# Performance work log

Measured on AMD Instinct MI355X. Metric: run time of the kernel, lower is better.

## Reference

```python
import jax, jax.numpy as jnp
import numpy as np

N_NODES = 100000
N_EDGES = 1600000
F_IN, HIDDEN, N_CLS = 128, 128, 40


def _gcn_layer(h, W, b, src, dst, norm, n):
    # h: [n, d_in] -> linear transform then edge-normalized scatter-add
    h = h @ W                                   # [n, d_out]
    msg = h[src] * norm[:, None]                # gather over edges [E', d_out]
    out = jax.ops.segment_sum(msg, dst, num_segments=n)
    return out + b


def setup_inputs() -> dict:
    key = jax.random.key(0)
    k1, k2, k3, k4 = jax.random.split(key, 4)
    x = jax.random.normal(k1, (N_NODES, F_IN), dtype=jnp.float32)
    edge_index = jax.random.randint(k2, (2, N_EDGES), 0, N_NODES, dtype=jnp.int32)
    # glorot-style init
    W1 = jax.random.normal(k3, (F_IN, HIDDEN), dtype=jnp.float32) * (1.0 / np.sqrt(F_IN))
    W2 = jax.random.normal(k4, (HIDDEN, N_CLS), dtype=jnp.float32) * (1.0 / np.sqrt(HIDDEN))
    b1 = jnp.zeros((HIDDEN,), dtype=jnp.float32)
    b2 = jnp.zeros((N_CLS,), dtype=jnp.float32)
    return {"x": x, "edge_index": edge_index, "W1": W1, "b1": b1,
            "W2": W2, "b2": b2, "dropout": 0}


def reference(x, edge_index, W1, b1, W2, b2, dropout):
    n = x.shape[0]
    src, dst = edge_index[0], edge_index[1]
    # add self loops (PyG GCNConv default)
    loop = jnp.arange(n, dtype=src.dtype)
    src = jnp.concatenate([src, loop])
    dst = jnp.concatenate([dst, loop])
    # symmetric normalization D^{-1/2} (A+I) D^{-1/2}
    deg = jax.ops.segment_sum(jnp.ones(src.shape, dtype=x.dtype), dst, num_segments=n)
    dinv = jnp.where(deg > 0, jax.lax.rsqrt(deg), 0.0)
    norm = dinv[src] * dinv[dst]                # [E + n]
    h = jax.nn.relu(_gcn_layer(x, W1, b1, src, dst, norm, n))
    # F.dropout with training=False is identity (eval mode)
    return _gcn_layer(h, W2, b2, src, dst, norm, n)
```

## Files before the change

kernel.cpp:

```cpp
#include <hip/hip_runtime.h>
#include <stdint.h>


#define NF 128
#define NC 40
#define PSHIFT 7
#define PNODES 128
#define GH 256

typedef __attribute__((ext_vector_type(8))) short short8;
typedef __attribute__((ext_vector_type(4))) float float4m;

__device__ __forceinline__ float bflo2f(unsigned int u) {
  union { unsigned int i; float f; } v; v.i = u << 16; return v.f;
}
__device__ __forceinline__ float bfhi2f(unsigned int u) {
  union { unsigned int i; float f; } v; v.i = u & 0xffff0000u; return v.f;
}
__device__ __forceinline__ unsigned short f2bf(float f) {
  union { float f; unsigned int i; } v; v.f = f;
  unsigned int x = v.i;
  return (unsigned short)((x + 0x7fffu + ((x >> 16) & 1u)) >> 16);
}

__device__ __forceinline__ unsigned int rowld64(const unsigned int* __restrict__ B,
                                                int idx, int lane) {
  unsigned int off = ((unsigned)idx << 6) | (unsigned)lane;
  __builtin_assume(off < (1u << 25));
  return B[off];
}
__device__ __forceinline__ unsigned int rowld20(const unsigned int* __restrict__ B,
                                                int idx, int ci) {
  unsigned int off = (unsigned)idx * 20u + (unsigned)ci;
  __builtin_assume(off < (1u << 22));
  return B[off];
}
__device__ __forceinline__ int4 bidx4(const int4* __restrict__ B, int off) {
  __builtin_assume(off >= 0 && off < (1 << 22));
  return B[off];
}

__global__ __launch_bounds__(256) void hist_pack_k(
    const int* __restrict__ ei, int* __restrict__ histT, int E, int CPB, int NPART,
    const float* __restrict__ W1, const float* __restrict__ W2,
    unsigned short* __restrict__ Bpack, unsigned short* __restrict__ W2pack,
    unsigned int* __restrict__ Hsu, unsigned int* __restrict__ H2u, int n) {
  int tid = threadIdx.x, bid = blockIdx.x;
  if (bid >= GH) {
    int g = (bid - GH) * 256 + tid;
    const float* W; unsigned short* dst; int cols, frag;
    if (g < 2048)      { W = W1; dst = Bpack;  cols = 128; frag = g; }
    else if (g < 2816) { W = W2; dst = W2pack; cols = 40;  frag = g - 2048; }
    else if (g < 2880) { Hsu[(size_t)n * 64 + (g - 2816)] = 0u; return; }
    else if (g < 2900) { H2u[(size_t)n * 20 + (g - 2880)] = 0u; return; }
    else return;
    int ct = frag >> 8, ks = (frag >> 6) & 3, lane = frag & 63;
    int quad = lane >> 4, l15 = lane & 15;
    int col = ct * 16 + l15, krow = ks * 32 + quad * 8;
    ushort4 lo = {0,0,0,0}, hi = {0,0,0,0};
    if (col < cols) {
      lo.x = f2bf(W[(krow + 0) * cols + col]);
      lo.y = f2bf(W[(krow + 1) * cols + col]);
      lo.z = f2bf(W[(krow + 2) * cols + col]);
      lo.w = f2bf(W[(krow + 3) * cols + col]);
      hi.x = f2bf(W[(krow + 4) * cols + col]);
      hi.y = f2bf(W[(krow + 5) * cols + col]);
      hi.z = f2bf(W[(krow + 6) * cols + col]);
      hi.w = f2bf(W[(krow + 7) * cols + col]);
    }
    *(ushort4*)&dst[(size_t)frag * 8 + 0] = lo;
    *(ushort4*)&dst[(size_t)frag * 8 + 4] = hi;
    return;
  }
  __shared__ int h[1024];
  for (int i = tid; i < NPART; i += 256) h[i] = 0;
  __syncthreads();
  int e0 = bid * CPB, e1 = min(e0 + CPB, E);
  for (int e = e0 + tid; e < e1; e += 256)
    atomicAdd(&h[ei[E + e] >> PSHIFT], 1);
  __syncthreads();
  for (int i = tid; i < NPART; i += 256) histT[(size_t)i * GH + bid] = h[i];
}

__global__ __launch_bounds__(256) void scanA_k(int* __restrict__ histT,
                                               int* __restrict__ partTotal) {
  __shared__ int sm[GH];
  int tid = threadIdx.x, p = blockIdx.x;
  int v = histT[(size_t)p * GH + tid];
  sm[tid] = v; __syncthreads();
  for (int off = 1; off < GH; off <<= 1) {
    int t = (tid >= off) ? sm[tid - off] : 0;
    __syncthreads();
    sm[tid] += t;
    __syncthreads();
  }
  histT[(size_t)p * GH + tid] = sm[tid] - v;
  if (tid == GH - 1) partTotal[p] = sm[GH - 1];
}

__global__ __launch_bounds__(1024) void scanB_k(const int* __restrict__ partTotal,
                                                int* __restrict__ base, int NPART) {
  __shared__ int sm[1024];
  int tid = threadIdx.x;
  int v = (tid < NPART) ? partTotal[tid] : 0;
  sm[tid] = v; __syncthreads();
  for (int off = 1; off < 1024; off <<= 1) {
    int t = (tid >= off) ? sm[tid - off] : 0;
    __syncthreads();
    sm[tid] += t;
    __syncthreads();
  }
  if (tid < NPART) base[tid] = sm[tid] - v;
}

__global__ __launch_bounds__(256) void scatter_k(const int* __restrict__ ei,
                                                 const int* __restrict__ histT,
                                                 const int* __restrict__ base,
                                                 unsigned int* __restrict__ epart,
                                                 int E, int CPB, int NPART) {
  __shared__ int off[1024];
  int tid = threadIdx.x, bid = blockIdx.x;
  for (int i = tid; i < NPART; i += 256)
    off[i] = base[i] + histT[(size_t)i * GH + bid];
  __syncthreads();
  int e0 = bid * CPB, e1 = min(e0 + CPB, E);
  for (int e = e0 + tid; e < e1; e += 256) {
    int s = ei[e], d = ei[E + e];
    int pos = atomicAdd(&off[d >> PSHIFT], 1);
    epart[pos] = ((unsigned int)(d & (PNODES - 1)) << 25) | (unsigned int)s;
  }
}

__global__ __launch_bounds__(256) void degpart_k(const unsigned int* __restrict__ epart,
                                                 const int* __restrict__ base,
                                                 const int* __restrict__ partTotal,
                                                 int* __restrict__ deg,
                                                 float* __restrict__ dinv, int n) {
  __shared__ int lcnt[PNODES];
  int tid = threadIdx.x, p = blockIdx.x;
  if (tid < PNODES) lcnt[tid] = 0;
  __syncthreads();
  int st = base[p], m = partTotal[p];
  for (int e = tid; e < m; e += 256)
    atomicAdd(&lcnt[epart[(size_t)st + e] >> 25], 1);
  __syncthreads();
  int node = (p << PSHIFT) + tid;
  if (tid < PNODES && node < n) {
    int c = lcnt[tid];
    deg[node] = c;
    dinv[node] = rsqrtf((float)c + 1.0f);
  }
}

__global__ __launch_bounds__(256) void build_gemm_k(
    const float* __restrict__ x, const unsigned short* __restrict__ Bpack,
    unsigned short* __restrict__ Hs, const unsigned int* __restrict__ epart,
    const int* __restrict__ base, const int* __restrict__ partTotal,
    const float* __restrict__ dinv,
    int* __restrict__ bucket, int n, int NPART, int G1) {
  __shared__ alignas(16) char smem[50176];
  int tid = threadIdx.x, bid = blockIdx.x;

  if (bid % 3 == 2) {
    int pidx = bid / 3;
    if (pidx >= NPART) return;
    int* lcnt = (int*)smem;
    int* lbuck = lcnt + PNODES;
    if (tid < PNODES) lcnt[tid] = 0;
    __syncthreads();
    int st = base[pidx], m = partTotal[pidx];
    for (int e = tid; e < m; e += 256) {
      unsigned int u = epart[(size_t)st + e];
      int ln = (int)(u >> 25), s = (int)(u & 0x1ffffffu);
      int pos = atomicAdd(&lcnt[ln], 1);
      if (pos < 64) lbuck[ln * 64 + pos] = s;
    }
    __syncthreads();
    int node0 = pidx << PSHIFT;
    int nn = min(PNODES, n - node0);
    for (int i = tid; i < nn; i += 256) {
      int c = lcnt[i]; if (c > 64) c = 64;
      int c8 = (c + 7) & ~7; if (c8 > 64) c8 = 64;
      for (int p = c; p < c8; p++) lbuck[i * 64 + p] = n;
    }
    __syncthreads();
    int4* bg = (int4*)&bucket[(size_t)node0 * 64];
    const int4* bl = (const int4*)lbuck;
    for (int i = tid; i < nn * 16; i += 256) {
      int nd = i >> 4, q = i & 15;
      int c = lcnt[nd]; if (c > 64) c = 64;
      int c8 = (c + 7) & ~7; if (c8 > 64) c8 = 64;
      if (q * 4 < c8) bg[i] = bl[i];
    }
    return;
  }

  int idx = (bid / 3) * 2 + (bid % 3);
  if (idx >= G1) return;
  unsigned short* As = (unsigned short*)smem;
  unsigned short* Bs = (unsigned short*)(smem + 17408);
  int r0 = idx * 64;

  const float4* x4 = (const float4*)x;
  for (int i = tid; i < 2048; i += 256) {
    int kc = i & 31, r = i >> 5;
    float4 v = make_float4(0.f, 0.f, 0.f, 0.f);
    if (r0 + r < n) {
      float dr = dinv[r0 + r];
      v = x4[(size_t)(r0 + r) * 32 + kc];
      v.x *= dr; v.y *= dr; v.z *= dr; v.w *= dr;
    }
    ushort4 o;
    o.x = f2bf(v.x); o.y = f2bf(v.y); o.z = f2bf(v.z); o.w = f2bf(v.w);
    *(ushort4*)&As[r * 136 + kc * 4] = o;
  }
  {
    const uint4* bp4 = (const uint4*)Bpack;
    uint4* bs4 = (uint4*)Bs;
    for (int i = tid; i < 2048; i += 256) bs4[i] = bp4[i];
  }
  __syncthreads();

  int wv = tid >> 6, lane = tid & 63;
  int quad = lane >> 4, l15 = lane & 15;

  short8 afr[4];
#pragma unroll
  for (int ks = 0; ks < 4; ks++)
    afr[ks] = *(const short8*)&As[(wv * 16 + l15) * 136 + ks * 32 + quad * 8];

  float4m acc[8];
#pragma unroll
  for (int i = 0; i < 8; i++) acc[i] = (float4m){0.f, 0.f, 0.f, 0.f};

#pragma unroll
  for (int ct = 0; ct < 8; ct++) {
#pragma unroll
    for (int ks = 0; ks < 4; ks++) {
      short8 bfr = *(const short8*)&Bs[(((ct * 4 + ks) * 64) + lane) * 8];
      acc[ct] = __builtin_amdgcn_mfma_f32_16x16x32_bf16(afr[ks], bfr, acc[ct], 0, 0, 0);
    }
  }

  __syncthreads();
  unsigned short* Cs = (unsigned short*)smem;
  int rloc = wv * 16 + quad * 4;
#pragma unroll
  for (int ct = 0; ct < 8; ct++) {
#pragma unroll
    for (int reg = 0; reg < 4; reg++)
      Cs[(rloc + reg) * 128 + ct * 16 + l15] = f2bf(acc[ct][reg]);
  }
  __syncthreads();
  uint4* HsV = (uint4*)Hs;
  const uint4* CsV = (const uint4*)Cs;
  for (int i = tid; i < 1024; i += 256) {
    int r = i >> 4;
    if (r0 + r < n) HsV[(size_t)(r0 + r) * 16 + (i & 15)] = CsV[i];
  }
}

__global__ __launch_bounds__(256, 8) void agg1f_k(const unsigned int* __restrict__ Hs2,
                                               const int* __restrict__ deg,
                                               const int* __restrict__ bucket,
                                               const float* __restrict__ dinv,
                                               const float2* __restrict__ b1v,
                                               const unsigned short* __restrict__ W2pack,
                                               unsigned short* __restrict__ H2s, int n) {
  __shared__ unsigned short As[16 * 136];
  __shared__ unsigned short W2s[768 * 8];
  int tid = threadIdx.x, wv = tid >> 6, lane = tid & 63;
  int node0 = blockIdx.x * 16;

  {
    const uint4* p = (const uint4*)W2pack;
    uint4* q = (uint4*)W2s;
    for (int i = tid; i < 768; i += 256) q[i] = p[i];
  }

  float2 bv = b1v[lane];
  const int4* bucket4 = (const int4*)bucket;

  for (int s = 0; s < 4; s++) {
    int mrow = wv * 4 + s;
    int node = node0 + mrow;
    float r0 = 0.f, r1 = 0.f;
    if (node < n) {
      float d = dinv[node];
      unsigned int v = rowld64(Hs2, node, lane);
      float a0 = bflo2f(v), a1 = bfhi2f(v);
      int m = deg[node]; if (m > 64) m = 64;
      int m8 = (m + 7) & ~7;
      int bq0 = node * 16;
      int p = 0;
      for (; p + 15 < m8; p += 16) {
        int4 qa = bidx4(bucket4, bq0 + (p >> 2) + 0);
        int4 qb = bidx4(bucket4, bq0 + (p >> 2) + 1);
        int4 qc = bidx4(bucket4, bq0 + (p >> 2) + 2);
        int4 qd = bidx4(bucket4, bq0 + (p >> 2) + 3);
        unsigned int u0  = rowld64(Hs2, qa.x, lane);
        unsigned int u1  = rowld64(Hs2, qa.y, lane);
        unsigned int u2  = rowld64(Hs2, qa.z, lane);
        unsigned int u3  = rowld64(Hs2, qa.w, lane);
        unsigned int u4  = rowld64(Hs2, qb.x, lane);
        unsigned int u5  = rowld64(Hs2, qb.y, lane);
        unsigned int u6  = rowld64(Hs2, qb.z, lane);
        unsigned int u7  = rowld64(Hs2, qb.w, lane);
        unsigned int u8  = rowld64(Hs2, qc.x, lane);
        unsigned int u9  = rowld64(Hs2, qc.y, lane);
        unsigned int u10 = rowld64(Hs2, qc.z, lane);
        unsigned int u11 = rowld64(Hs2, qc.w, lane);
        unsigned int u12 = rowld64(Hs2, qd.x, lane);
        unsigned int u13 = rowld64(Hs2, qd.y, lane);
        unsigned int u14 = rowld64(Hs2, qd.z, lane);
        unsigned int u15 = rowld64(Hs2, qd.w, lane);
        a0 += bflo2f(u0)  + bflo2f(u1)  + bflo2f(u2)  + bflo2f(u3)
            + bflo2f(u4)  + bflo2f(u5)  + bflo2f(u6)  + bflo2f(u7)
            + bflo2f(u8)  + bflo2f(u9)  + bflo2f(u10) + bflo2f(u11)
            + bflo2f(u12) + bflo2f(u13) + bflo2f(u14) + bflo2f(u15);
        a1 += bfhi2f(u0)  + bfhi2f(u1)  + bfhi2f(u2)  + bfhi2f(u3)
            + bfhi2f(u4)  + bfhi2f(u5)  + bfhi2f(u6)  + bfhi2f(u7)
            + bfhi2f(u8)  + bfhi2f(u9)  + bfhi2f(u10) + bfhi2f(u11)
            + bfhi2f(u12) + bfhi2f(u13) + bfhi2f(u14) + bfhi2f(u15);
      }
      if (p < m8) {
        int4 qa = bidx4(bucket4, bq0 + (p >> 2) + 0);
        int4 qb = bidx4(bucket4, bq0 + (p >> 2) + 1);
        unsigned int u0 = rowld64(Hs2, qa.x, lane);
        unsigned int u1 = rowld64(Hs2, qa.y, lane);
        unsigned int u2 = rowld64(Hs2, qa.z, lane);
        unsigned int u3 = rowld64(Hs2, qa.w, lane);
        unsigned int u4 = rowld64(Hs2, qb.x, lane);
        unsigned int u5 = rowld64(Hs2, qb.y, lane);
        unsigned int u6 = rowld64(Hs2, qb.z, lane);
        unsigned int u7 = rowld64(Hs2, qb.w, lane);
        a0 += bflo2f(u0) + bflo2f(u1) + bflo2f(u2) + bflo2f(u3)
            + bflo2f(u4) + bflo2f(u5) + bflo2f(u6) + bflo2f(u7);
        a1 += bfhi2f(u0) + bfhi2f(u1) + bfhi2f(u2) + bfhi2f(u3)
            + bfhi2f(u4) + bfhi2f(u5) + bfhi2f(u6) + bfhi2f(u7);
      }
      r0 = fmaxf(0.0f, bv.x + d * a0);
      r1 = fmaxf(0.0f, bv.y + d * a1);
    }
    unsigned int pk = (unsigned int)f2bf(r0) | ((unsigned int)f2bf(r1) << 16);
    *(unsigned int*)&As[mrow * 136 + lane * 2] = pk;
  }
  __syncthreads();

  if (wv < 3) {
    int quad = lane >> 4, l15 = lane & 15;
    float4m acc = (float4m){0.f, 0.f, 0.f, 0.f};
#pragma unroll
    for (int ks = 0; ks < 4; ks++) {
      short8 afr = *(const short8*)&As[l15 * 136 + ks * 32 + quad * 8];
      short8 bfr = *(const short8*)&W2s[(((wv * 4 + ks) * 64) + lane) * 8];
      acc = __builtin_amdgcn_mfma_f32_16x16x32_bf16(afr, bfr, acc, 0, 0, 0);
    }
    int c = wv * 16 + l15;
    if (c < NC) {
#pragma unroll
      for (int reg = 0; reg < 4; reg++) {
        int node = node0 + quad * 4 + reg;
        if (node < n) {
          float dd = dinv[node];
          H2s[(size_t)node * 40 + c] = f2bf(acc[reg] * dd);
        }
      }
    }
  }
}

__global__ __launch_bounds__(256) void agg2_k(const unsigned int* __restrict__ H2u,
                                              const int* __restrict__ deg,
                                              const int* __restrict__ bucket,
                                              const float* __restrict__ dinv,
                                              const float* __restrict__ b2,
                                              float* __restrict__ outp, int n) {
  int w = (blockIdx.x * 256 + threadIdx.x) >> 6;
  int lane = threadIdx.x & 63;
  int sub = lane / 20, ci = lane - sub * 20;
  int node = w * 3 + sub;
  if (sub >= 3 || node >= n) return;

  float d = dinv[node];
  unsigned int u = rowld20(H2u, node, ci);
  float a0 = bflo2f(u), a1 = bfhi2f(u);

  int m = deg[node]; if (m > 64) m = 64;
  int m8 = (m + 7) & ~7;
  const int4* bucket4 = (const int4*)bucket;
  int bq0 = node * 16;
  for (int p = 0; p < m8; p += 8) {
    int4 qa = bidx4(bucket4, bq0 + (p >> 2) + 0);
    int4 qb = bidx4(bucket4, bq0 + (p >> 2) + 1);
    unsigned int u0 = rowld20(H2u, qa.x, ci);
    unsigned int u1 = rowld20(H2u, qa.y, ci);
    unsigned int u2 = rowld20(H2u, qa.z, ci);
    unsigned int u3 = rowld20(H2u, qa.w, ci);
    unsigned int u4 = rowld20(H2u, qb.x, ci);
    unsigned int u5 = rowld20(H2u, qb.y, ci);
    unsigned int u6 = rowld20(H2u, qb.z, ci);
    unsigned int u7 = rowld20(H2u, qb.w, ci);
    a0 += bflo2f(u0)+bflo2f(u1)+bflo2f(u2)+bflo2f(u3)
        + bflo2f(u4)+bflo2f(u5)+bflo2f(u6)+bflo2f(u7);
    a1 += bfhi2f(u0)+bfhi2f(u1)+bfhi2f(u2)+bfhi2f(u3)
        + bfhi2f(u4)+bfhi2f(u5)+bfhi2f(u6)+bfhi2f(u7);
  }

  float2 o;
  o.x = b2[2 * ci]     + d * a0;
  o.y = b2[2 * ci + 1] + d * a1;
  *(float2*)&outp[(size_t)node * 40 + 2 * ci] = o;
}

extern "C" void kernel_launch(void* const* d_in, const int* in_sizes, int n_in,
                              void* d_out, int out_size, void* d_ws, size_t ws_size,
                              hipStream_t stream) {
  const float* x  = (const float*)d_in[0];
  const int*   ei = (const int*)d_in[1];
  const float* W1 = (const float*)d_in[2];
  const float* b1 = (const float*)d_in[3];
  const float* W2 = (const float*)d_in[4];
  const float* b2 = (const float*)d_in[5];

  int N = in_sizes[0] / NF;
  int E = in_sizes[1] / 2;
  int NPART = (N + PNODES - 1) >> PSHIFT;
  int CPB = (E + GH - 1) / GH;
  int G1 = (N + 63) / 64;

  char* ws = (char*)d_ws;
  size_t off = 0;
  auto carve = [&](size_t bytes) {
    void* p = ws + off;
    off += (bytes + 255) & ~(size_t)255;
    return p;
  };
  int*            deg       = (int*)carve((size_t)N * 4);
  float*          dinv      = (float*)carve((size_t)N * 4);
  int*            bucket    = (int*)carve((size_t)N * 64 * 4);
  unsigned short* Hs        = (unsigned short*)carve((size_t)(N + 1) * NF * 2);
  int*            histT     = (int*)carve((size_t)NPART * GH * 4);
  int*            partTotal = (int*)carve((size_t)NPART * 4);
  int*            base      = (int*)carve((size_t)NPART * 4);
  unsigned int*   epart     = (unsigned int*)carve((size_t)E * 4);
  unsigned short* Bpack     = (unsigned short*)carve(2048 * 8 * 2);
  unsigned short* W2pack    = (unsigned short*)carve(768 * 8 * 2);
  unsigned short* H2s       = (unsigned short*)carve((size_t)(N + 1) * NC * 2);

  hist_pack_k<<<GH + 12, 256, 0, stream>>>(ei, histT, E, CPB, NPART,
                                           W1, W2, Bpack, W2pack,
                                           (unsigned int*)Hs, (unsigned int*)H2s, N);
  scanA_k<<<NPART, 256, 0, stream>>>(histT, partTotal);
  scanB_k<<<1, 1024, 0, stream>>>(partTotal, base, NPART);
  scatter_k<<<GH, 256, 0, stream>>>(ei, histT, base, epart, E, CPB, NPART);
  degpart_k<<<NPART, 256, 0, stream>>>(epart, base, partTotal, deg, dinv, N);
  build_gemm_k<<<3 * NPART, 256, 0, stream>>>(x, Bpack, Hs, epart, base, partTotal,
                                              dinv, bucket, N, NPART, G1);
  agg1f_k<<<(N + 15) / 16, 256, 0, stream>>>((const unsigned int*)Hs, deg, bucket,
                                             dinv, (const float2*)b1, W2pack, H2s, N);
  int NW = (N + 2) / 3;
  agg2_k<<<((size_t)NW * 64 + 255) / 256, 256, 0, stream>>>((const unsigned int*)H2s,
                                                            deg, bucket, dinv, b2,
                                                            (float*)d_out, N);
}
```

Baseline: 252.1 us.

## Pad layer-2 feature rows to 64 bf16 and unroll aggregation by 16

Layer-2 hidden rows grow from a 40-element to a 64-element bf16 stride, so row offsets become a shift and each gathered row starts on a 128-byte boundary. The second aggregation loop now processes 16 neighbors per iteration, with an 8-neighbor tail, so more gathers are in flight at once. The cost is a larger intermediate buffer with padding that is never read, and higher register pressure in the aggregation kernel.

```diff
diff --git a/kernel.cpp b/kernel.cpp
--- a/kernel.cpp
+++ b/kernel.cpp
@@ -29,10 +29,10 @@
   __builtin_assume(off < (1u << 25));
   return B[off];
 }
-__device__ __forceinline__ unsigned int rowld20(const unsigned int* __restrict__ B,
+__device__ __forceinline__ unsigned int rowld32(const unsigned int* __restrict__ B,
                                                 int idx, int ci) {
-  unsigned int off = (unsigned)idx * 20u + (unsigned)ci;
-  __builtin_assume(off < (1u << 22));
+  unsigned int off = ((unsigned)idx << 5) | (unsigned)ci;
+  __builtin_assume(off < (1u << 23));
   return B[off];
 }
 __device__ __forceinline__ int4 bidx4(const int4* __restrict__ B, int off) {
@@ -52,7 +52,7 @@
     if (g < 2048)      { W = W1; dst = Bpack;  cols = 128; frag = g; }
     else if (g < 2816) { W = W2; dst = W2pack; cols = 40;  frag = g - 2048; }
     else if (g < 2880) { Hsu[(size_t)n * 64 + (g - 2816)] = 0u; return; }
-    else if (g < 2900) { H2u[(size_t)n * 20 + (g - 2880)] = 0u; return; }
+    else if (g < 2912) { H2u[(size_t)n * 32 + (g - 2880)] = 0u; return; }
     else return;
     int ct = frag >> 8, ks = (frag >> 6) & 3, lane = frag & 63;
     int quad = lane >> 4, l15 = lane & 15;
@@ -363,7 +363,7 @@
         int node = node0 + quad * 4 + reg;
         if (node < n) {
           float dd = dinv[node];
-          H2s[(size_t)node * 40 + c] = f2bf(acc[reg] * dd);
+          H2s[(size_t)node * 64 + c] = f2bf(acc[reg] * dd);
         }
       }
     }
@@ -383,24 +383,55 @@
   if (sub >= 3 || node >= n) return;
 
   float d = dinv[node];
-  unsigned int u = rowld20(H2u, node, ci);
+  unsigned int u = rowld32(H2u, node, ci);
   float a0 = bflo2f(u), a1 = bfhi2f(u);
 
   int m = deg[node]; if (m > 64) m = 64;
   int m8 = (m + 7) & ~7;
   const int4* bucket4 = (const int4*)bucket;
   int bq0 = node * 16;
-  for (int p = 0; p < m8; p += 8) {
+  int p = 0;
+  for (; p + 15 < m8; p += 16) {
     int4 qa = bidx4(bucket4, bq0 + (p >> 2) + 0);
     int4 qb = bidx4(bucket4, bq0 + (p >> 2) + 1);
-    unsigned int u0 = rowld20(H2u, qa.x, ci);
-    unsigned int u1 = rowld20(H2u, qa.y, ci);
-    unsigned int u2 = rowld20(H2u, qa.z, ci);
-    unsigned int u3 = rowld20(H2u, qa.w, ci);
-    unsigned int u4 = rowld20(H2u, qb.x, ci);
-    unsigned int u5 = rowld20(H2u, qb.y, ci);
-    unsigned int u6 = rowld20(H2u, qb.z, ci);
-    unsigned int u7 = rowld20(H2u, qb.w, ci);
+    int4 qc = bidx4(bucket4, bq0 + (p >> 2) + 2);
+    int4 qd = bidx4(bucket4, bq0 + (p >> 2) + 3);
+    unsigned int u0  = rowld32(H2u, qa.x, ci);
+    unsigned int u1  = rowld32(H2u, qa.y, ci);
+    unsigned int u2  = rowld32(H2u, qa.z, ci);
+    unsigned int u3  = rowld32(H2u, qa.w, ci);
+    unsigned int u4  = rowld32(H2u, qb.x, ci);
+    unsigned int u5  = rowld32(H2u, qb.y, ci);
+    unsigned int u6  = rowld32(H2u, qb.z, ci);
+    unsigned int u7  = rowld32(H2u, qb.w, ci);
+    unsigned int u8  = rowld32(H2u, qc.x, ci);
+    unsigned int u9  = rowld32(H2u, qc.y, ci);
+    unsigned int u10 = rowld32(H2u, qc.z, ci);
+    unsigned int u11 = rowld32(H2u, qc.w, ci);
+    unsigned int u12 = rowld32(H2u, qd.x, ci);
+    unsigned int u13 = rowld32(H2u, qd.y, ci);
+    unsigned int u14 = rowld32(H2u, qd.z, ci);
+    unsigned int u15 = rowld32(H2u, qd.w, ci);
+    a0 += bflo2f(u0) +bflo2f(u1) +bflo2f(u2) +bflo2f(u3)
+        + bflo2f(u4) +bflo2f(u5) +bflo2f(u6) +bflo2f(u7)
+        + bflo2f(u8) +bflo2f(u9) +bflo2f(u10)+bflo2f(u11)
+        + bflo2f(u12)+bflo2f(u13)+bflo2f(u14)+bflo2f(u15);
+    a1 += bfhi2f(u0) +bfhi2f(u1) +bfhi2f(u2) +bfhi2f(u3)
+        + bfhi2f(u4) +bfhi2f(u5) +bfhi2f(u6) +bfhi2f(u7)
+        + bfhi2f(u8) +bfhi2f(u9) +bfhi2f(u10)+bfhi2f(u11)
+        + bfhi2f(u12)+bfhi2f(u13)+bfhi2f(u14)+bfhi2f(u15);
+  }
+  if (p < m8) {
+    int4 qa = bidx4(bucket4, bq0 + (p >> 2) + 0);
+    int4 qb = bidx4(bucket4, bq0 + (p >> 2) + 1);
+    unsigned int u0 = rowld32(H2u, qa.x, ci);
+    unsigned int u1 = rowld32(H2u, qa.y, ci);
+    unsigned int u2 = rowld32(H2u, qa.z, ci);
+    unsigned int u3 = rowld32(H2u, qa.w, ci);
+    unsigned int u4 = rowld32(H2u, qb.x, ci);
+    unsigned int u5 = rowld32(H2u, qb.y, ci);
+    unsigned int u6 = rowld32(H2u, qb.z, ci);
+    unsigned int u7 = rowld32(H2u, qb.w, ci);
     a0 += bflo2f(u0)+bflo2f(u1)+bflo2f(u2)+bflo2f(u3)
         + bflo2f(u4)+bflo2f(u5)+bflo2f(u6)+bflo2f(u7);
     a1 += bfhi2f(u0)+bfhi2f(u1)+bfhi2f(u2)+bfhi2f(u3)
@@ -446,7 +477,7 @@
   unsigned int*   epart     = (unsigned int*)carve((size_t)E * 4);
   unsigned short* Bpack     = (unsigned short*)carve(2048 * 8 * 2);
   unsigned short* W2pack    = (unsigned short*)carve(768 * 8 * 2);
-  unsigned short* H2s       = (unsigned short*)carve((size_t)(N + 1) * NC * 2);
+  unsigned short* H2s       = (unsigned short*)carve((size_t)(N + 1) * 64 * 2);
 
   hist_pack_k<<<GH + 12, 256, 0, stream>>>(ei, histT, E, CPB, NPART,
                                            W1, W2, Bpack, W2pack,
```

Result: no change. 253.0 us (+0.4%).
